# Performance work log

Measured on AMD Instinct MI355X. Metric: run time of the kernel, lower is better.

## Reference

```python
import jax, jax.numpy as jnp
import numpy as np

EPS = 1e-8

def _div(a, b, eps=EPS):
    # torch: a / (b*(b>eps) + (b<=eps)*eps)
    return a / jnp.where(b > eps, b, eps)

def _cos_lastdim(a, b, eps=EPS):
    # F.cosine_similarity(a, b, dim=-1): dot / (max(|a|,eps)*max(|b|,eps))
    dot = jnp.sum(a * b, axis=-1)
    na = jnp.sqrt(jnp.sum(a * a, axis=-1))
    nb = jnp.sqrt(jnp.sum(b * b, axis=-1))
    return dot / (jnp.maximum(na, eps) * jnp.maximum(nb, eps))

def _full_matching(q1, q2, w):
    # q1,q2: [b,s,h]; w: [p,h] -> [b,s,p]
    q1w = q1[:, :, None, :] * w            # [b,s,p,h]
    q2w = q2[:, :, None, :] * w
    return _cos_lastdim(q1w, q2w)

def _max_pool_matching(q1, q2, w, eps=EPS):
    # q1: [b,s1,h]; q2: [b,s2,h]; w: [p,h] -> [b,s1,p]
    q1w = q1[:, :, None, :] * w            # [b,s1,p,h]
    q2w = q2[:, :, None, :] * w            # [b,s2,p,h]
    dots = jnp.einsum('biph,bjph->bijp', q1w, q2w)   # [b,s1,s2,p]
    n1 = jnp.maximum(jnp.sqrt(jnp.sum(q1w * q1w, -1)), eps)  # [b,s1,p]
    n2 = jnp.maximum(jnp.sqrt(jnp.sum(q2w * q2w, -1)), eps)  # [b,s2,p]
    cos = dots / (n1[:, :, None, :] * n2[:, None, :, :])
    return jnp.max(cos, axis=2)            # max over s2

def _attention(q1, q2):
    # cosine attention matrix [b,s1,s2]
    n1 = jnp.sqrt(jnp.sum(q1 * q1, -1, keepdims=True))           # [b,s1,1]
    n2 = jnp.sqrt(jnp.sum(q2 * q2, -1, keepdims=True))           # [b,s2,1]
    mol = jnp.einsum('bih,bjh->bij', q1, q2)
    return _div(mol, n1 * n2.transpose(0, 2, 1))

def setup_inputs() -> dict:
    key = jax.random.key(0)
    k1, k2, k3 = jax.random.split(key, 3)
    q1_batch = jax.random.normal(k1, (16, 128, 512), dtype=jnp.float32)
    q2_batch = jax.random.normal(k2, (16, 192, 512), dtype=jnp.float32)
    W = jax.random.normal(k3, (8, 4, 256), dtype=jnp.float32)
    return {"q1_batch": q1_batch, "q2_batch": q2_batch, "W": W}

def reference(q1_batch, q2_batch, W):
    half = q1_batch.shape[-1] // 2
    s1 = q1_batch.shape[1]
    q1_fw, q1_bw = q1_batch[..., :half], q1_batch[..., half:]
    q2_fw, q2_bw = q2_batch[..., :half], q2_batch[..., half:]

    # 1) full matching against q2 last (fw) / first (bw) state
    q2_last = jnp.broadcast_to(q2_fw[:, -1:, :], q1_fw.shape)
    q2_first = jnp.broadcast_to(q2_bw[:, :1, :], q1_bw.shape)
    full_fw = _full_matching(q1_fw, q2_last, W[0])
    full_bw = _full_matching(q1_bw, q2_first, W[1])

    # 2) max-pool matching
    max_fw = _max_pool_matching(q1_fw, q2_fw, W[2])
    max_bw = _max_pool_matching(q1_bw, q2_bw, W[3])

    # 3) attentive matching
    att_fw = _attention(q1_fw, q2_fw)   # [b,s1,s2]
    att_bw = _attention(q1_bw, q2_bw)
    attened_q2_fw = att_fw[:, :, :, None] * q2_fw[:, None, :, :]  # [b,s1,s2,h]
    attened_q2_bw = att_bw[:, :, :, None] * q2_bw[:, None, :, :]
    mean_fw = _div(attened_q2_fw.sum(axis=2), att_fw.sum(axis=2, keepdims=True))
    mean_bw = _div(attened_q2_bw.sum(axis=2), att_bw.sum(axis=2, keepdims=True))
    att_match_fw = _full_matching(q1_fw, mean_fw, W[4])
    att_match_bw = _full_matching(q1_bw, mean_bw, W[5])

    # 4) max-attentive matching
    maxatt_q2_fw = jnp.max(attened_q2_fw, axis=2)  # [b,s1,h]
    maxatt_q2_bw = jnp.max(attened_q2_bw, axis=2)
    maxatt_fw = _full_matching(q1_fw, maxatt_q2_fw, W[6])
    maxatt_bw = _full_matching(q1_bw, maxatt_q2_bw, W[7])

    return jnp.concatenate(
        [full_fw, full_bw, max_fw, max_bw,
         att_match_fw, att_match_bw, maxatt_fw, maxatt_bw], axis=-1)
```

## Files before the change

### kernel.cpp

```cpp
#include <hip/hip_runtime.h>
#include <math.h>
#include <stdint.h>

#define NB 16
#define S1 128
#define S2 192
#define HH 256
#define PP 4
#define FULLH 512
#define EPSV 1e-8f

typedef float f32x4 __attribute__((ext_vector_type(4)));
typedef float f32x2 __attribute__((ext_vector_type(2)));
typedef short short8 __attribute__((ext_vector_type(8)));

#define WS_N2    0
#define WS_N2W   6144
#define WS_N1    30720
#define WS_N1W   34816
#define WS_Q2BF  919552
#define WS_Q2BFR 1705984
#define WS_N1X   2492416
#define WS_RVN   2541568
#define WS_Q1BF  2541696

__device__ __forceinline__ float dot4(const float4& a, const float4& b) {
    return a.x * b.x + a.y * b.y + a.z * b.z + a.w * b.w;
}

__device__ __forceinline__ float vdot4(const f32x4& a, const f32x4& b) {
    return a.x * b.x + a.y * b.y + a.z * b.z + a.w * b.w;
}

__device__ __forceinline__ uint16_t f2bf(float x) {
    union { float f; uint32_t u; } a;
    a.f = x;
    uint32_t r = a.u + 0x7FFF + ((a.u >> 16) & 1);
    return (uint16_t)(r >> 16);
}

__device__ __forceinline__ uint32_t pk2(float a, float b) {
    return (uint32_t)f2bf(a) | ((uint32_t)f2bf(b) << 16);
}

template<int N>
__device__ __forceinline__ void wave_reduce_sum_n(float* v) {
#pragma unroll
    for (int m = 1; m < 64; m <<= 1) {
#pragma unroll
        for (int i = 0; i < N; i++) v[i] += __shfl_xor(v[i], m, 64);
    }
}

__global__ __launch_bounds__(256) void norms_kernel(const float* __restrict__ q1,
                                                    const float* __restrict__ q2,
                                                    const float* __restrict__ W,
                                                    float* __restrict__ ws) {
    const int NQ2 = 2 * NB * S2;
    const int NQ1 = 2 * NB * S1;
    int gwid = (int)((blockIdx.x * blockDim.x + threadIdx.x) >> 6);
    int lane = threadIdx.x & 63;
    if (gwid >= NQ2 + NQ1) return;

    int h0 = lane * 4;
    int sg = lane >> 3;
    int khalf = (lane >> 1) & 3;
    int elo = (lane & 1) * 4;

    if (gwid < NQ2) {
        int d = gwid / (NB * S2);
        int rem = gwid - d * (NB * S2);
        int b_ = rem / S2;
        int j_ = rem - b_ * S2;
        int db = d * NB + b_;
        const float* row = q2 + ((size_t)(b_ * S2 + j_)) * FULLH + d * HH;
        float4 v = *reinterpret_cast<const float4*>(row + h0);
        const float* wmax = W + (size_t)(2 + d) * PP * HH;

        float s[5];
        s[0] = dot4(v, v);
#pragma unroll
        for (int p = 0; p < PP; p++) {
            float4 wv = *reinterpret_cast<const float4*>(wmax + p * HH + h0);
            float4 t;
            t.x = v.x * wv.x; t.y = v.y * wv.y; t.z = v.z * wv.z; t.w = v.w * wv.w;
            s[1 + p] = dot4(t, t);
        }
        wave_reduce_sum_n<5>(s);
        int nidx = db * S2 + j_;
        if (lane == 0) {
            ws[WS_N2 + nidx] = sqrtf(s[0]);
#pragma unroll
            for (int p = 0; p < PP; p++)
                ws[WS_N2W + (size_t)nidx * PP + p] = sqrtf(s[1 + p]);
        }

        if ((d == 0 && j_ == S2 - 1) || (d == 1 && j_ == 0)) {
            float e[4];
#pragma unroll
            for (int p = 0; p < PP; p++) {
                float4 wv = *reinterpret_cast<const float4*>(W + ((size_t)d * PP + p) * HH + h0);
                float4 t;
                t.x = v.x * wv.x; t.y = v.y * wv.y; t.z = v.z * wv.z; t.w = v.w * wv.w;
                e[p] = dot4(t, t);
            }
            wave_reduce_sum_n<4>(e);
            if (lane == 0) {
#pragma unroll
                for (int p = 0; p < PP; p++)
                    ws[WS_RVN + db * 4 + p] = sqrtf(e[p]);
            }
        }

        uint2 pk;
        pk.x = pk2(v.x, v.y);
        pk.y = pk2(v.z, v.w);
        {
            uint16_t* q2bf = (uint16_t*)(ws + WS_Q2BF) + (size_t)db * (S2 * HH);
            int jt = j_ >> 4, jcol = j_ & 15;
            size_t off = ((size_t)(jt * 8 + sg) * 64 + (khalf << 4) + jcol) * 8 + elo;
            *reinterpret_cast<uint2*>(q2bf + off) = pk;
        }
        {
            uint16_t* q2r = (uint16_t*)(ws + WS_Q2BFR) + ((size_t)db * S2 + j_) * HH;
            *reinterpret_cast<uint2*>(q2r + h0) = pk;
        }
    } else {
        int idx = gwid - NQ2;
        int d = idx >> 11;
        int b = (idx >> 7) & 15;
        int i = idx & 127;
        int db = d * NB + b;
        const float* row = q1 + ((size_t)(b * S1 + i)) * FULLH + d * HH;
        float4 v = *reinterpret_cast<const float4*>(row + h0);

        int banks[4] = {2 + d, d, 4 + d, 6 + d};
        float s[17];
        float4 y[4];
        s[0] = dot4(v, v);
#pragma unroll
        for (int t = 0; t < 4; t++) {
#pragma unroll
            for (int p = 0; p < PP; p++) {
                float4 wv = *reinterpret_cast<const float4*>(
                    W + ((size_t)banks[t] * PP + p) * HH + h0);
                float4 tv;
                tv.x = v.x * wv.x; tv.y = v.y * wv.y;
                tv.z = v.z * wv.z; tv.w = v.w * wv.w;
                s[1 + t * 4 + p] = dot4(tv, tv);
                if (t == 0) {
                    y[p].x = tv.x * wv.x; y[p].y = tv.y * wv.y;
                    y[p].z = tv.z * wv.z; y[p].w = tv.w * wv.w;
                }
            }
        }
        wave_reduce_sum_n<17>(s);
        if (lane == 0) {
            ws[WS_N1 + idx] = sqrtf(s[0]);
#pragma unroll
            for (int p = 0; p < PP; p++)
                ws[WS_N1W + (size_t)idx * PP + p] = sqrtf(s[1 + p]);
#pragma unroll
            for (int t = 0; t < 3; t++)
#pragma unroll
                for (int p = 0; p < PP; p++)
                    ws[WS_N1X + (size_t)idx * 12 + t * 4 + p] = sqrtf(s[5 + t * 4 + p]);
        }

        uint16_t* q1b5 = (uint16_t*)(ws + WS_Q1BF) + (size_t)db * 163840;
        int itile = i >> 4, icol = i & 15;
        size_t slot = (size_t)((khalf << 4) + icol) * 8 + elo;
        {
            uint2 pk;
            pk.x = pk2(v.x, v.y);
            pk.y = pk2(v.z, v.w);
            size_t so = ((size_t)(0 * 8 + itile) * 8 + sg) * 512 + slot;
            *reinterpret_cast<uint2*>(q1b5 + so) = pk;
        }
#pragma unroll
        for (int p = 0; p < PP; p++) {
            uint2 pk;
            pk.x = pk2(y[p].x, y[p].y);
            pk.y = pk2(y[p].z, y[p].w);
            size_t so = ((size_t)((p + 1) * 8 + itile) * 8 + sg) * 512 + slot;
            *reinterpret_cast<uint2*>(q1b5 + so) = pk;
        }
    }
}

__global__ __launch_bounds__(256) void sapply_kernel(const float* __restrict__ q1,
                                                     const float* __restrict__ q2,
                                                     const float* __restrict__ W,
                                                     const float* __restrict__ ws,
                                                     float* __restrict__ out) {
    __shared__ float att_s[S2][8];
    __shared__ float satt_s[4][8];
    __shared__ float mc_s[4][8][4];

    int bid = blockIdx.x;
    int xcd = bid & 7;
    int rest = bid >> 3;
    int db = xcd + 8 * (rest & 3);
    int it8 = rest >> 2;
    int d = db >> 4;
    int b = db & 15;
    int itile = it8 >> 1;
    int half = it8 & 1;

    int tid = threadIdx.x;
    int w = tid >> 6;
    int lane = tid & 63;
    int h0 = lane * 4;

    {
        int jq = w;
        const uint16_t* q2bfp = (const uint16_t*)(ws + WS_Q2BF) + (size_t)db * (S2 * HH);
        const uint16_t* q1bfp = (const uint16_t*)(ws + WS_Q1BF) + (size_t)db * 163840;

        f32x4 acc[5][3];
#pragma unroll
        for (int v = 0; v < 5; v++)
#pragma unroll
            for (int jt_i = 0; jt_i < 3; jt_i++) acc[v][jt_i] = (f32x4){0.f, 0.f, 0.f, 0.f};

#pragma unroll
        for (int kc = 0; kc < 4; kc++) {
            short8 Bf[3][2];
#pragma unroll
            for (int jt_i = 0; jt_i < 3; jt_i++)
#pragma unroll
                for (int sl = 0; sl < 2; sl++)
                    Bf[jt_i][sl] = *reinterpret_cast<const short8*>(
                        q2bfp + ((size_t)((jq * 3 + jt_i) * 8 + kc * 2 + sl) * 64 + lane) * 8);
#pragma unroll
            for (int v = 0; v < 5; v++) {
                short8 A0 = *reinterpret_cast<const short8*>(
                    q1bfp + ((size_t)(v * 8 + itile) * 8 + kc * 2 + 0) * 512 + lane * 8);
                short8 A1 = *reinterpret_cast<const short8*>(
                    q1bfp + ((size_t)(v * 8 + itile) * 8 + kc * 2 + 1) * 512 + lane * 8);
#pragma unroll
                for (int jt_i = 0; jt_i < 3; jt_i++) {
                    acc[v][jt_i] = __builtin_amdgcn_mfma_f32_16x16x32_bf16(A0, Bf[jt_i][0], acc[v][jt_i], 0, 0, 0);
                    acc[v][jt_i] = __builtin_amdgcn_mfma_f32_16x16x32_bf16(A1, Bf[jt_i][1], acc[v][jt_i], 0, 0, 0);
                }
            }
        }

        int lhi = lane >> 4;
        int lcol = lane & 15;
        bool keep = (lhi >> 1) == half;
        int ii0 = (lhi & 1) * 4;
        int nbase = db * S2;
        int q1b_ = db * S1 + itile * 16 + lhi * 4;

        float n1v[4], n1wc[4][4];
#pragma unroll
        for (int rr = 0; rr < 4; rr++) {
            n1v[rr] = ws[WS_N1 + q1b_ + rr];
#pragma unroll
            for (int p = 0; p < 4; p++)
                n1wc[rr][p] = fmaxf(ws[WS_N1W + (size_t)(q1b_ + rr) * 4 + p], EPSV);
        }

        float satt_acc[4] = {0.f, 0.f, 0.f, 0.f};
        float mc_acc[4][4];
#pragma unroll
        for (int p = 0; p < 4; p++)
#pragma unroll
            for (int rr = 0; rr < 4; rr++) mc_acc[p][rr] = -INFINITY;

#pragma unroll
        for (int jt_i = 0; jt_i < 3; jt_i++) {
            int j = (jq * 3 + jt_i) * 16 + lcol;
            float n2 = ws[WS_N2 + nbase + j];
            float avv[4];
#pragma unroll
            for (int rr = 0; rr < 4; rr++) {
                float den = n1v[rr] * n2;
                avv[rr] = acc[0][jt_i][rr] / (den > EPSV ? den : EPSV);
                satt_acc[rr] += avv[rr];
            }
            if (keep) {
                float4 av;
                av.x = avv[0]; av.y = avv[1]; av.z = avv[2]; av.w = avv[3];
                *reinterpret_cast<float4*>(&att_s[j][ii0]) = av;
            }
#pragma unroll
            for (int p = 0; p < 4; p++) {
                float n2wv = fmaxf(ws[WS_N2W + (size_t)(nbase + j) * 4 + p], EPSV);
#pragma unroll
                for (int rr = 0; rr < 4; rr++) {
                    float cosv = acc[p + 1][jt_i][rr] / (n1wc[rr][p] * n2wv);
                    mc_acc[p][rr] = fmaxf(mc_acc[p][rr], cosv);
                }
            }
        }

#pragma unroll
        for (int m = 1; m < 16; m <<= 1) {
#pragma unroll
            for (int rr = 0; rr < 4; rr++) satt_acc[rr] += __shfl_xor(satt_acc[rr], m, 64);
#pragma unroll
            for (int p = 0; p < 4; p++)
#pragma unroll
                for (int rr = 0; rr < 4; rr++)
                    mc_acc[p][rr] = fmaxf(mc_acc[p][rr], __shfl_xor(mc_acc[p][rr], m, 64));
        }
        if (keep && lcol == 0) {
#pragma unroll
            for (int rr = 0; rr < 4; rr++) {
                satt_s[jq][ii0 + rr] = satt_acc[rr];
#pragma unroll
                for (int p = 0; p < 4; p++)
                    mc_s[jq][ii0 + rr][p] = mc_acc[p][rr];
            }
        }
    }
    __syncthreads();

    {
        const uint16_t* q2r = (const uint16_t*)(ws + WS_Q2BFR) + (size_t)db * S2 * HH;
        int il0 = w * 2;
        int i0 = it8 * 8 + il0;

        f32x4 macc0 = (f32x4){0.f, 0.f, 0.f, 0.f};
        f32x4 macc1 = (f32x4){0.f, 0.f, 0.f, 0.f};
        f32x4 mx0 = (f32x4){-INFINITY, -INFINITY, -INFINITY, -INFINITY};
        f32x4 mx1 = (f32x4){-INFINITY, -INFINITY, -INFINITY, -INFINITY};

#pragma unroll 8
        for (int j = 0; j < S2; j++) {
            uint2 u = *reinterpret_cast<const uint2*>(q2r + (size_t)j * HH + h0);
            f32x2 a2 = *reinterpret_cast<const f32x2*>(&att_s[j][il0]);
            union { uint32_t u; float f; } c0, c1, c2, c3;
            c0.u = u.x << 16; c1.u = u.x & 0xFFFF0000u;
            c2.u = u.y << 16; c3.u = u.y & 0xFFFF0000u;
            f32x4 qv = (f32x4){c0.f, c1.f, c2.f, c3.f};
            f32x4 a0 = (f32x4){a2.x, a2.x, a2.x, a2.x};
            f32x4 a1 = (f32x4){a2.y, a2.y, a2.y, a2.y};
            macc0 = __builtin_elementwise_fma(a0, qv, macc0);
            macc1 = __builtin_elementwise_fma(a1, qv, macc1);
            mx0 = __builtin_elementwise_max(mx0, a0 * qv);
            mx1 = __builtin_elementwise_max(mx1, a1 * qv);
        }

        float satt0 = satt_s[0][il0] + satt_s[1][il0] + satt_s[2][il0] + satt_s[3][il0];
        float satt1 = satt_s[0][il0 + 1] + satt_s[1][il0 + 1] +
                      satt_s[2][il0 + 1] + satt_s[3][il0 + 1];
        float sden0 = satt0 > EPSV ? satt0 : EPSV;
        float sden1 = satt1 > EPSV ? satt1 : EPSV;

        if (lane < 8) {
            int iw = il0 + (lane >> 2);
            int p = lane & 3;
            float m = fmaxf(fmaxf(mc_s[0][iw][p], mc_s[1][iw][p]),
                            fmaxf(mc_s[2][iw][p], mc_s[3][iw][p]));
            out[((size_t)(b * S1 + it8 * 8 + iw)) * 32 + 8 + 4 * d + p] = m;
        }

        f32x4 mean0 = macc0 * (1.0f / sden0);
        f32x4 mean1 = macc1 * (1.0f / sden1);
        f32x4 rv = *reinterpret_cast<const f32x4*>(
            q2 + (size_t)b * S2 * FULLH + d * HH +
            (d == 0 ? (size_t)(S2 - 1) * FULLH : (size_t)0) + h0);
        f32x4 q1v0 = *reinterpret_cast<const f32x4*>(
            q1 + ((size_t)(b * S1 + i0)) * FULLH + d * HH + h0);
        f32x4 q1v1 = *reinterpret_cast<const f32x4*>(
            q1 + ((size_t)(b * S1 + i0 + 1)) * FULLH + d * HH + h0);

        f32x4 q1rv0 = q1v0 * rv, q1me0 = q1v0 * mean0, me20 = mean0 * mean0;
        f32x4 q1mx0 = q1v0 * mx0, mx20 = mx0 * mx0;
        f32x4 q1rv1 = q1v1 * rv, q1me1 = q1v1 * mean1, me21 = mean1 * mean1;
        f32x4 q1mx1 = q1v1 * mx1, mx21 = mx1 * mx1;

        float s[40];
#pragma unroll
        for (int p = 0; p < 4; p++) {
            f32x4 wf = *reinterpret_cast<const f32x4*>(W + ((size_t)d * PP + p) * HH + h0);
            f32x4 wa = *reinterpret_cast<const f32x4*>(W + ((size_t)(4 + d) * PP + p) * HH + h0);
            f32x4 wm = *reinterpret_cast<const f32x4*>(W + ((size_t)(6 + d) * PP + p) * HH + h0);
            f32x4 w2f = wf * wf, w2a = wa * wa, w2m = wm * wm;
            s[p * 5 + 0] = vdot4(q1rv0, w2f);
            s[p * 5 + 1] = vdot4(q1me0, w2a);
            s[p * 5 + 2] = vdot4(me20, w2a);
            s[p * 5 + 3] = vdot4(q1mx0, w2m);
            s[p * 5 + 4] = vdot4(mx20, w2m);
            s[20 + p * 5 + 0] = vdot4(q1rv1, w2f);
            s[20 + p * 5 + 1] = vdot4(q1me1, w2a);
            s[20 + p * 5 + 2] = vdot4(me21, w2a);
            s[20 + p * 5 + 3] = vdot4(q1mx1, w2m);
            s[20 + p * 5 + 4] = vdot4(mx21, w2m);
        }
        wave_reduce_sum_n<40>(s);

        if (lane == 0) {
#pragma unroll
            for (int ii = 0; ii < 2; ii++) {
                int i = i0 + ii;
                int qi = db * S1 + i;
                size_t obase = ((size_t)(b * S1 + i)) * 32;
                const float* nx = ws + WS_N1X + (size_t)qi * 12;
#pragma unroll
                for (int p = 0; p < 4; p++) {
                    float nf = fmaxf(nx[p], EPSV);
                    float na = fmaxf(nx[4 + p], EPSV);
                    float nm = fmaxf(nx[8 + p], EPSV);
                    float rvn = fmaxf(ws[WS_RVN + db * 4 + p], EPSV);
                    const float* sp = s + ii * 20 + p * 5;
                    out[obase + 0 + 4 * d + p] = sp[0] / (nf * rvn);
                    out[obase + 16 + 4 * d + p] = sp[1] / (na * fmaxf(sqrtf(sp[2]), EPSV));
                    out[obase + 24 + 4 * d + p] = sp[3] / (nm * fmaxf(sqrtf(sp[4]), EPSV));
                }
            }
        }
    }
}

extern "C" void kernel_launch(void* const* d_in, const int* in_sizes, int n_in,
                              void* d_out, int out_size, void* d_ws, size_t ws_size,
                              hipStream_t stream) {
    const float* q1 = (const float*)d_in[0];
    const float* q2 = (const float*)d_in[1];
    const float* W = (const float*)d_in[2];
    float* out = (float*)d_out;
    float* ws = (float*)d_ws;

    int nrows = 2 * NB * S2 + 2 * NB * S1;
    int nblocks_norm = (nrows * 64 + 255) / 256;
    norms_kernel<<<dim3(nblocks_norm), dim3(256), 0, stream>>>(q1, q2, W, ws);

    sapply_kernel<<<dim3(512), dim3(256), 0, stream>>>(q1, q2, W, ws, out);
}
```

Baseline: 53.91 us.

## Fuse norm/bf16-packing prepass into main kernel, computing norms and conversions inline

Removes the separate norms kernel and its workspace round-trip. The main kernel now loads fp32 q1/q2 rows directly, computes squared norms and weighted norms while building bf16 MFMA fragments in registers, and reduces them with cross-lane shuffles. The attention pass reads fp32 q2 instead of a bf16 copy, and the full-matching norms are folded into the final wave reduction. This saves one launch and the workspace writes and reads, in exchange for redundant conversion and norm work across blocks that share the same rows, plus extra register pressure.

```diff
diff --git a/kernel.cpp b/kernel.cpp
--- a/kernel.cpp
+++ b/kernel.cpp
@@ -14,33 +14,29 @@
 typedef float f32x2 __attribute__((ext_vector_type(2)));
 typedef short short8 __attribute__((ext_vector_type(8)));
 
-#define WS_N2    0
-#define WS_N2W   6144
-#define WS_N1    30720
-#define WS_N1W   34816
-#define WS_Q2BF  919552
-#define WS_Q2BFR 1705984
-#define WS_N1X   2492416
-#define WS_RVN   2541568
-#define WS_Q1BF  2541696
-
-__device__ __forceinline__ float dot4(const float4& a, const float4& b) {
-    return a.x * b.x + a.y * b.y + a.z * b.z + a.w * b.w;
-}
-
 __device__ __forceinline__ float vdot4(const f32x4& a, const f32x4& b) {
     return a.x * b.x + a.y * b.y + a.z * b.z + a.w * b.w;
 }
 
-__device__ __forceinline__ uint16_t f2bf(float x) {
+__device__ __forceinline__ uint32_t f2bfu(float x) {
     union { float f; uint32_t u; } a;
     a.f = x;
-    uint32_t r = a.u + 0x7FFF + ((a.u >> 16) & 1);
-    return (uint16_t)(r >> 16);
+    return a.u + 0x7FFF + ((a.u >> 16) & 1);
 }
 
 __device__ __forceinline__ uint32_t pk2(float a, float b) {
-    return (uint32_t)f2bf(a) | ((uint32_t)f2bf(b) << 16);
+    return (f2bfu(a) >> 16) | (f2bfu(b) & 0xFFFF0000u);
+}
+
+union bf8pack { uint32_t u[4]; short8 s; };
+
+__device__ __forceinline__ short8 cvt8(const f32x4& a, const f32x4& b) {
+    bf8pack p;
+    p.u[0] = pk2(a.x, a.y);
+    p.u[1] = pk2(a.z, a.w);
+    p.u[2] = pk2(b.x, b.y);
+    p.u[3] = pk2(b.z, b.w);
+    return p.s;
 }
 
 template<int N>
@@ -52,147 +48,10 @@
     }
 }
 
-__global__ __launch_bounds__(256) void norms_kernel(const float* __restrict__ q1,
+__global__ __launch_bounds__(256) void fused_kernel(const float* __restrict__ q1,
                                                     const float* __restrict__ q2,
                                                     const float* __restrict__ W,
-                                                    float* __restrict__ ws) {
-    const int NQ2 = 2 * NB * S2;
-    const int NQ1 = 2 * NB * S1;
-    int gwid = (int)((blockIdx.x * blockDim.x + threadIdx.x) >> 6);
-    int lane = threadIdx.x & 63;
-    if (gwid >= NQ2 + NQ1) return;
-
-    int h0 = lane * 4;
-    int sg = lane >> 3;
-    int khalf = (lane >> 1) & 3;
-    int elo = (lane & 1) * 4;
-
-    if (gwid < NQ2) {
-        int d = gwid / (NB * S2);
-        int rem = gwid - d * (NB * S2);
-        int b_ = rem / S2;
-        int j_ = rem - b_ * S2;
-        int db = d * NB + b_;
-        const float* row = q2 + ((size_t)(b_ * S2 + j_)) * FULLH + d * HH;
-        float4 v = *reinterpret_cast<const float4*>(row + h0);
-        const float* wmax = W + (size_t)(2 + d) * PP * HH;
-
-        float s[5];
-        s[0] = dot4(v, v);
-#pragma unroll
-        for (int p = 0; p < PP; p++) {
-            float4 wv = *reinterpret_cast<const float4*>(wmax + p * HH + h0);
-            float4 t;
-            t.x = v.x * wv.x; t.y = v.y * wv.y; t.z = v.z * wv.z; t.w = v.w * wv.w;
-            s[1 + p] = dot4(t, t);
-        }
-        wave_reduce_sum_n<5>(s);
-        int nidx = db * S2 + j_;
-        if (lane == 0) {
-            ws[WS_N2 + nidx] = sqrtf(s[0]);
-#pragma unroll
-            for (int p = 0; p < PP; p++)
-                ws[WS_N2W + (size_t)nidx * PP + p] = sqrtf(s[1 + p]);
-        }
-
-        if ((d == 0 && j_ == S2 - 1) || (d == 1 && j_ == 0)) {
-            float e[4];
-#pragma unroll
-            for (int p = 0; p < PP; p++) {
-                float4 wv = *reinterpret_cast<const float4*>(W + ((size_t)d * PP + p) * HH + h0);
-                float4 t;
-                t.x = v.x * wv.x; t.y = v.y * wv.y; t.z = v.z * wv.z; t.w = v.w * wv.w;
-                e[p] = dot4(t, t);
-            }
-            wave_reduce_sum_n<4>(e);
-            if (lane == 0) {
-#pragma unroll
-                for (int p = 0; p < PP; p++)
-                    ws[WS_RVN + db * 4 + p] = sqrtf(e[p]);
-            }
-        }
-
-        uint2 pk;
-        pk.x = pk2(v.x, v.y);
-        pk.y = pk2(v.z, v.w);
-        {
-            uint16_t* q2bf = (uint16_t*)(ws + WS_Q2BF) + (size_t)db * (S2 * HH);
-            int jt = j_ >> 4, jcol = j_ & 15;
-            size_t off = ((size_t)(jt * 8 + sg) * 64 + (khalf << 4) + jcol) * 8 + elo;
-            *reinterpret_cast<uint2*>(q2bf + off) = pk;
-        }
-        {
-            uint16_t* q2r = (uint16_t*)(ws + WS_Q2BFR) + ((size_t)db * S2 + j_) * HH;
-            *reinterpret_cast<uint2*>(q2r + h0) = pk;
-        }
-    } else {
-        int idx = gwid - NQ2;
-        int d = idx >> 11;
-        int b = (idx >> 7) & 15;
-        int i = idx & 127;
-        int db = d * NB + b;
-        const float* row = q1 + ((size_t)(b * S1 + i)) * FULLH + d * HH;
-        float4 v = *reinterpret_cast<const float4*>(row + h0);
-
-        int banks[4] = {2 + d, d, 4 + d, 6 + d};
-        float s[17];
-        float4 y[4];
-        s[0] = dot4(v, v);
-#pragma unroll
-        for (int t = 0; t < 4; t++) {
-#pragma unroll
-            for (int p = 0; p < PP; p++) {
-                float4 wv = *reinterpret_cast<const float4*>(
-                    W + ((size_t)banks[t] * PP + p) * HH + h0);
-                float4 tv;
-                tv.x = v.x * wv.x; tv.y = v.y * wv.y;
-                tv.z = v.z * wv.z; tv.w = v.w * wv.w;
-                s[1 + t * 4 + p] = dot4(tv, tv);
-                if (t == 0) {
-                    y[p].x = tv.x * wv.x; y[p].y = tv.y * wv.y;
-                    y[p].z = tv.z * wv.z; y[p].w = tv.w * wv.w;
-                }
-            }
-        }
-        wave_reduce_sum_n<17>(s);
-        if (lane == 0) {
-            ws[WS_N1 + idx] = sqrtf(s[0]);
-#pragma unroll
-            for (int p = 0; p < PP; p++)
-                ws[WS_N1W + (size_t)idx * PP + p] = sqrtf(s[1 + p]);
-#pragma unroll
-            for (int t = 0; t < 3; t++)
-#pragma unroll
-                for (int p = 0; p < PP; p++)
-                    ws[WS_N1X + (size_t)idx * 12 + t * 4 + p] = sqrtf(s[5 + t * 4 + p]);
-        }
-
-        uint16_t* q1b5 = (uint16_t*)(ws + WS_Q1BF) + (size_t)db * 163840;
-        int itile = i >> 4, icol = i & 15;
-        size_t slot = (size_t)((khalf << 4) + icol) * 8 + elo;
-        {
-            uint2 pk;
-            pk.x = pk2(v.x, v.y);
-            pk.y = pk2(v.z, v.w);
-            size_t so = ((size_t)(0 * 8 + itile) * 8 + sg) * 512 + slot;
-            *reinterpret_cast<uint2*>(q1b5 + so) = pk;
-        }
-#pragma unroll
-        for (int p = 0; p < PP; p++) {
-            uint2 pk;
-            pk.x = pk2(y[p].x, y[p].y);
-            pk.y = pk2(y[p].z, y[p].w);
-            size_t so = ((size_t)((p + 1) * 8 + itile) * 8 + sg) * 512 + slot;
-            *reinterpret_cast<uint2*>(q1b5 + so) = pk;
-        }
-    }
-}
-
-__global__ __launch_bounds__(256) void sapply_kernel(const float* __restrict__ q1,
-                                                     const float* __restrict__ q2,
-                                                     const float* __restrict__ W,
-                                                     const float* __restrict__ ws,
-                                                     float* __restrict__ out) {
+                                                    float* __restrict__ out) {
     __shared__ float att_s[S2][8];
     __shared__ float satt_s[4][8];
     __shared__ float mc_s[4][8][4];
@@ -211,38 +70,86 @@
     int w = tid >> 6;
     int lane = tid & 63;
     int h0 = lane * 4;
+    int row = lane & 15;
+    int kg = lane >> 4;
+
+    const float* q2b = q2 + (size_t)b * S2 * FULLH + d * HH;
+    const float* q1t = q1 + ((size_t)(b * S1 + itile * 16 + row)) * FULLH + d * HH;
+    const float* wmax = W + (size_t)(2 + d) * PP * HH;
+    int jq = w;
 
     {
-        int jq = w;
-        const uint16_t* q2bfp = (const uint16_t*)(ws + WS_Q2BF) + (size_t)db * (S2 * HH);
-        const uint16_t* q1bfp = (const uint16_t*)(ws + WS_Q1BF) + (size_t)db * 163840;
-
         f32x4 acc[5][3];
 #pragma unroll
         for (int v = 0; v < 5; v++)
 #pragma unroll
             for (int jt_i = 0; jt_i < 3; jt_i++) acc[v][jt_i] = (f32x4){0.f, 0.f, 0.f, 0.f};
 
-#pragma unroll
+        float n1a = 0.f, n1wa[4] = {0.f, 0.f, 0.f, 0.f};
+        float n2a[3] = {0.f, 0.f, 0.f};
+        float n2wa[3][4];
+#pragma unroll
+        for (int jt_i = 0; jt_i < 3; jt_i++)
+#pragma unroll
+            for (int p = 0; p < 4; p++) n2wa[jt_i][p] = 0.f;
+
         for (int kc = 0; kc < 4; kc++) {
-            short8 Bf[3][2];
-#pragma unroll
-            for (int jt_i = 0; jt_i < 3; jt_i++)
-#pragma unroll
-                for (int sl = 0; sl < 2; sl++)
-                    Bf[jt_i][sl] = *reinterpret_cast<const short8*>(
-                        q2bfp + ((size_t)((jq * 3 + jt_i) * 8 + kc * 2 + sl) * 64 + lane) * 8);
-#pragma unroll
-            for (int v = 0; v < 5; v++) {
-                short8 A0 = *reinterpret_cast<const short8*>(
-                    q1bfp + ((size_t)(v * 8 + itile) * 8 + kc * 2 + 0) * 512 + lane * 8);
-                short8 A1 = *reinterpret_cast<const short8*>(
-                    q1bfp + ((size_t)(v * 8 + itile) * 8 + kc * 2 + 1) * 512 + lane * 8);
+#pragma unroll
+            for (int sl = 0; sl < 2; sl++) {
+                int hb = kc * 64 + sl * 32 + kg * 8;
+                f32x4 w2a[4], w2b[4];
+#pragma unroll
+                for (int p = 0; p < 4; p++) {
+                    f32x4 wa = *reinterpret_cast<const f32x4*>(wmax + p * HH + hb);
+                    f32x4 wb = *reinterpret_cast<const f32x4*>(wmax + p * HH + hb + 4);
+                    w2a[p] = wa * wa;
+                    w2b[p] = wb * wb;
+                }
+                short8 Af[5];
+                {
+                    f32x4 xa = *reinterpret_cast<const f32x4*>(q1t + hb);
+                    f32x4 xb = *reinterpret_cast<const f32x4*>(q1t + hb + 4);
+                    n1a += vdot4(xa, xa) + vdot4(xb, xb);
+                    Af[0] = cvt8(xa, xb);
+#pragma unroll
+                    for (int p = 0; p < 4; p++) {
+                        f32x4 ya = xa * w2a[p];
+                        f32x4 yb = xb * w2b[p];
+                        n1wa[p] += vdot4(ya, xa) + vdot4(yb, xb);
+                        Af[p + 1] = cvt8(ya, yb);
+                    }
+                }
 #pragma unroll
                 for (int jt_i = 0; jt_i < 3; jt_i++) {
-                    acc[v][jt_i] = __builtin_amdgcn_mfma_f32_16x16x32_bf16(A0, Bf[jt_i][0], acc[v][jt_i], 0, 0, 0);
-                    acc[v][jt_i] = __builtin_amdgcn_mfma_f32_16x16x32_bf16(A1, Bf[jt_i][1], acc[v][jt_i], 0, 0, 0);
-                }
+                    int j = (jq * 3 + jt_i) * 16 + row;
+                    f32x4 ba = *reinterpret_cast<const f32x4*>(q2b + (size_t)j * FULLH + hb);
+                    f32x4 bb = *reinterpret_cast<const f32x4*>(q2b + (size_t)j * FULLH + hb + 4);
+                    f32x4 bsa = ba * ba, bsb = bb * bb;
+                    n2a[jt_i] += (bsa.x + bsa.y + bsa.z + bsa.w) +
+                                 (bsb.x + bsb.y + bsb.z + bsb.w);
+#pragma unroll
+                    for (int p = 0; p < 4; p++)
+                        n2wa[jt_i][p] += vdot4(bsa, w2a[p]) + vdot4(bsb, w2b[p]);
+                    short8 Bf = cvt8(ba, bb);
+#pragma unroll
+                    for (int v = 0; v < 5; v++)
+                        acc[v][jt_i] = __builtin_amdgcn_mfma_f32_16x16x32_bf16(
+                            Af[v], Bf, acc[v][jt_i], 0, 0, 0);
+                }
+            }
+        }
+
+#pragma unroll
+        for (int m = 16; m <= 32; m <<= 1) {
+            n1a += __shfl_xor(n1a, m, 64);
+#pragma unroll
+            for (int p = 0; p < 4; p++) n1wa[p] += __shfl_xor(n1wa[p], m, 64);
+#pragma unroll
+            for (int jt_i = 0; jt_i < 3; jt_i++) {
+                n2a[jt_i] += __shfl_xor(n2a[jt_i], m, 64);
+#pragma unroll
+                for (int p = 0; p < 4; p++)
+                    n2wa[jt_i][p] += __shfl_xor(n2wa[jt_i][p], m, 64);
             }
         }
 
@@ -250,16 +157,14 @@
         int lcol = lane & 15;
         bool keep = (lhi >> 1) == half;
         int ii0 = (lhi & 1) * 4;
-        int nbase = db * S2;
-        int q1b_ = db * S1 + itile * 16 + lhi * 4;
 
         float n1v[4], n1wc[4][4];
 #pragma unroll
         for (int rr = 0; rr < 4; rr++) {
-            n1v[rr] = ws[WS_N1 + q1b_ + rr];
+            n1v[rr] = sqrtf(__shfl(n1a, lhi * 4 + rr, 64));
 #pragma unroll
             for (int p = 0; p < 4; p++)
-                n1wc[rr][p] = fmaxf(ws[WS_N1W + (size_t)(q1b_ + rr) * 4 + p], EPSV);
+                n1wc[rr][p] = fmaxf(sqrtf(__shfl(n1wa[p], lhi * 4 + rr, 64)), EPSV);
         }
 
         float satt_acc[4] = {0.f, 0.f, 0.f, 0.f};
@@ -272,7 +177,7 @@
 #pragma unroll
         for (int jt_i = 0; jt_i < 3; jt_i++) {
             int j = (jq * 3 + jt_i) * 16 + lcol;
-            float n2 = ws[WS_N2 + nbase + j];
+            float n2 = sqrtf(n2a[jt_i]);
             float avv[4];
 #pragma unroll
             for (int rr = 0; rr < 4; rr++) {
@@ -287,7 +192,7 @@
             }
 #pragma unroll
             for (int p = 0; p < 4; p++) {
-                float n2wv = fmaxf(ws[WS_N2W + (size_t)(nbase + j) * 4 + p], EPSV);
+                float n2wv = fmaxf(sqrtf(n2wa[jt_i][p]), EPSV);
 #pragma unroll
                 for (int rr = 0; rr < 4; rr++) {
                     float cosv = acc[p + 1][jt_i][rr] / (n1wc[rr][p] * n2wv);
@@ -319,7 +224,6 @@
     __syncthreads();
 
     {
-        const uint16_t* q2r = (const uint16_t*)(ws + WS_Q2BFR) + (size_t)db * S2 * HH;
         int il0 = w * 2;
         int i0 = it8 * 8 + il0;
 
@@ -330,12 +234,8 @@
 
 #pragma unroll 8
         for (int j = 0; j < S2; j++) {
-            uint2 u = *reinterpret_cast<const uint2*>(q2r + (size_t)j * HH + h0);
+            f32x4 qv = *reinterpret_cast<const f32x4*>(q2b + (size_t)j * FULLH + h0);
             f32x2 a2 = *reinterpret_cast<const f32x2*>(&att_s[j][il0]);
-            union { uint32_t u; float f; } c0, c1, c2, c3;
-            c0.u = u.x << 16; c1.u = u.x & 0xFFFF0000u;
-            c2.u = u.y << 16; c3.u = u.y & 0xFFFF0000u;
-            f32x4 qv = (f32x4){c0.f, c1.f, c2.f, c3.f};
             f32x4 a0 = (f32x4){a2.x, a2.x, a2.x, a2.x};
             f32x4 a1 = (f32x4){a2.y, a2.y, a2.y, a2.y};
             macc0 = __builtin_elementwise_fma(a0, qv, macc0);
@@ -361,8 +261,7 @@
         f32x4 mean0 = macc0 * (1.0f / sden0);
         f32x4 mean1 = macc1 * (1.0f / sden1);
         f32x4 rv = *reinterpret_cast<const f32x4*>(
-            q2 + (size_t)b * S2 * FULLH + d * HH +
-            (d == 0 ? (size_t)(S2 - 1) * FULLH : (size_t)0) + h0);
+            q2b + (d == 0 ? (size_t)(S2 - 1) * FULLH : (size_t)0) + h0);
         f32x4 q1v0 = *reinterpret_cast<const f32x4*>(
             q1 + ((size_t)(b * S1 + i0)) * FULLH + d * HH + h0);
         f32x4 q1v1 = *reinterpret_cast<const f32x4*>(
@@ -370,43 +269,51 @@
 
         f32x4 q1rv0 = q1v0 * rv, q1me0 = q1v0 * mean0, me20 = mean0 * mean0;
         f32x4 q1mx0 = q1v0 * mx0, mx20 = mx0 * mx0;
+        f32x4 q1sq0 = q1v0 * q1v0;
         f32x4 q1rv1 = q1v1 * rv, q1me1 = q1v1 * mean1, me21 = mean1 * mean1;
         f32x4 q1mx1 = q1v1 * mx1, mx21 = mx1 * mx1;
-
-        float s[40];
+        f32x4 q1sq1 = q1v1 * q1v1;
+        f32x4 rv2 = rv * rv;
+
+        float s[68];
 #pragma unroll
         for (int p = 0; p < 4; p++) {
             f32x4 wf = *reinterpret_cast<const f32x4*>(W + ((size_t)d * PP + p) * HH + h0);
             f32x4 wa = *reinterpret_cast<const f32x4*>(W + ((size_t)(4 + d) * PP + p) * HH + h0);
             f32x4 wm = *reinterpret_cast<const f32x4*>(W + ((size_t)(6 + d) * PP + p) * HH + h0);
             f32x4 w2f = wf * wf, w2a = wa * wa, w2m = wm * wm;
-            s[p * 5 + 0] = vdot4(q1rv0, w2f);
-            s[p * 5 + 1] = vdot4(q1me0, w2a);
-            s[p * 5 + 2] = vdot4(me20, w2a);
-            s[p * 5 + 3] = vdot4(q1mx0, w2m);
-            s[p * 5 + 4] = vdot4(mx20, w2m);
-            s[20 + p * 5 + 0] = vdot4(q1rv1, w2f);
-            s[20 + p * 5 + 1] = vdot4(q1me1, w2a);
-            s[20 + p * 5 + 2] = vdot4(me21, w2a);
-            s[20 + p * 5 + 3] = vdot4(q1mx1, w2m);
-            s[20 + p * 5 + 4] = vdot4(mx21, w2m);
-        }
-        wave_reduce_sum_n<40>(s);
+            s[p * 8 + 0] = vdot4(q1rv0, w2f);
+            s[p * 8 + 1] = vdot4(q1me0, w2a);
+            s[p * 8 + 2] = vdot4(me20, w2a);
+            s[p * 8 + 3] = vdot4(q1mx0, w2m);
+            s[p * 8 + 4] = vdot4(mx20, w2m);
+            s[p * 8 + 5] = vdot4(q1sq0, w2f);
+            s[p * 8 + 6] = vdot4(q1sq0, w2a);
+            s[p * 8 + 7] = vdot4(q1sq0, w2m);
+            s[32 + p * 8 + 0] = vdot4(q1rv1, w2f);
+            s[32 + p * 8 + 1] = vdot4(q1me1, w2a);
+            s[32 + p * 8 + 2] = vdot4(me21, w2a);
+            s[32 + p * 8 + 3] = vdot4(q1mx1, w2m);
+            s[32 + p * 8 + 4] = vdot4(mx21, w2m);
+            s[32 + p * 8 + 5] = vdot4(q1sq1, w2f);
+            s[32 + p * 8 + 6] = vdot4(q1sq1, w2a);
+            s[32 + p * 8 + 7] = vdot4(q1sq1, w2m);
+            s[64 + p] = vdot4(rv2, w2f);
+        }
+        wave_reduce_sum_n<68>(s);
 
         if (lane == 0) {
 #pragma unroll
             for (int ii = 0; ii < 2; ii++) {
                 int i = i0 + ii;
-                int qi = db * S1 + i;
                 size_t obase = ((size_t)(b * S1 + i)) * 32;
-                const float* nx = ws + WS_N1X + (size_t)qi * 12;
 #pragma unroll
                 for (int p = 0; p < 4; p++) {
-                    float nf = fmaxf(nx[p], EPSV);
-                    float na = fmaxf(nx[4 + p], EPSV);
-                    float nm = fmaxf(nx[8 + p], EPSV);
-                    float rvn = fmaxf(ws[WS_RVN + db * 4 + p], EPSV);
-                    const float* sp = s + ii * 20 + p * 5;
+                    const float* sp = s + ii * 32 + p * 8;
+                    float rvn = fmaxf(sqrtf(s[64 + p]), EPSV);
+                    float nf = fmaxf(sqrtf(sp[5]), EPSV);
+                    float na = fmaxf(sqrtf(sp[6]), EPSV);
+                    float nm = fmaxf(sqrtf(sp[7]), EPSV);
                     out[obase + 0 + 4 * d + p] = sp[0] / (nf * rvn);
                     out[obase + 16 + 4 * d + p] = sp[1] / (na * fmaxf(sqrtf(sp[2]), EPSV));
                     out[obase + 24 + 4 * d + p] = sp[3] / (nm * fmaxf(sqrtf(sp[4]), EPSV));
@@ -423,11 +330,6 @@
     const float* q2 = (const float*)d_in[1];
     const float* W = (const float*)d_in[2];
     float* out = (float*)d_out;
-    float* ws = (float*)d_ws;
-
-    int nrows = 2 * NB * S2 + 2 * NB * S1;
-    int nblocks_norm = (nrows * 64 + 255) / 256;
-    norms_kernel<<<dim3(nblocks_norm), dim3(256), 0, stream>>>(q1, q2, W, ws);
-
-    sapply_kernel<<<dim3(512), dim3(256), 0, stream>>>(q1, q2, W, ws, out);
-}
+
+    fused_kernel<<<dim3(512), dim3(256), 0, stream>>>(q1, q2, W, out);
+}
```

After: 81.94 us. 52.0% more time.
